# Kernel optimization log

Measured on AMD Instinct MI355X. Metric: run time of the kernel, lower is better.

## Reference

```python
import jax, jax.numpy as jnp
import numpy as np

M, H, D, P = 256, 32, 128, 4096
N = H * D
L = P + M  # total cache length after concat


def setup_inputs() -> dict:
    key = jax.random.key(0)
    ks = jax.random.split(key, 8)
    X = jax.random.normal(ks[0], (M, N), dtype=jnp.float32)
    # projection weights (nn.Linear stores [out, in]; y = x @ W.T)
    Wq = jax.random.normal(ks[1], (N, N), dtype=jnp.float32) * 0.005
    Wk = jax.random.normal(ks[2], (N, N), dtype=jnp.float32) * 0.005
    Wv = jax.random.normal(ks[3], (N, N), dtype=jnp.float32) * 0.005
    cache_K = jax.random.normal(ks[4], (H, P, D), dtype=jnp.float32) * 0.3
    cache_V = jax.random.normal(ks[5], (H, P, D), dtype=jnp.float32) * 0.3
    noise = jax.random.normal(ks[6], (H, M, L), dtype=jnp.float32) * 0.5
    tau = jnp.asarray(2.0, dtype=jnp.float32)
    return {"X": X, "Wq": Wq, "Wk": Wk, "Wv": Wv,
            "cache_K": cache_K, "cache_V": cache_V, "tau": tau, "noise": noise}


def reference(X, Wq, Wk, Wv, cache_K, cache_V, tau, noise):
    # project and split heads: [M, N] -> [H, M, D]
    q = (X @ Wq.T).reshape(M, H, D).transpose(1, 0, 2)
    k = (X @ Wk.T).reshape(M, H, D).transpose(1, 0, 2)
    v = (X @ Wv.T).reshape(M, H, D).transpose(1, 0, 2)
    k_cache = jnp.concatenate([cache_K, k], axis=1)  # [H, L, D]
    v_cache = jnp.concatenate([cache_V, v], axis=1)  # [H, L, D]
    c = jnp.einsum('hmd,hld->hml', q, k_cache)       # [H, M, L]
    # faithful to source: plain exp normalization (no max-subtract), twice
    c_exp = jnp.exp(c)
    c_exp_perturb = jnp.exp((c + noise) / tau)
    c_div = c_exp / jnp.sum(c_exp, axis=2, keepdims=True)
    c_div_perturb = c_exp_perturb / jnp.sum(c_exp_perturb, axis=2, keepdims=True)
    c_out = jnp.sum(c_div_perturb, axis=1)           # [H, L] token scores
    o = jnp.einsum('hml,hld->hmd', c_div, v_cache)   # [H, M, D]
    o2 = o.transpose(1, 0, 2).reshape(M, N)
    return o2, c_out
```

## Files before the change

### kernel.cpp

```cpp
#include <hip/hip_runtime.h>
#include <hip/hip_bf16.h>

#define MM 256
#define HH 32
#define DD 128
#define PP 4096
#define NN 4096
#define LL 4352
#define NSTR 8
#define SPL 4

typedef __attribute__((ext_vector_type(8))) short short8;
typedef __attribute__((ext_vector_type(4))) float f32x4;

__device__ __forceinline__ unsigned short f2bf(float f) {
    union { float f; unsigned u; } x; x.f = f;
    unsigned u = x.u;
    return (unsigned short)((u + 0x7fffu + ((u >> 16) & 1u)) >> 16);
}

__device__ __forceinline__ float bf2f(unsigned short u) {
    union { unsigned u; float f; } x; x.u = ((unsigned)u) << 16;
    return x.f;
}

__device__ __forceinline__ unsigned pkbf(float lo, float hi) {
    unsigned r;
    asm("v_cvt_pk_bf16_f32 %0, %1, %2" : "=v"(r) : "v"(lo), "v"(hi));
    return r;
}

__device__ __forceinline__ short8 pk8(float4 a, float4 b) {
    union { short8 s; unsigned u[4]; } o;
    o.u[0] = pkbf(a.x, a.y); o.u[1] = pkbf(a.z, a.w);
    o.u[2] = pkbf(b.x, b.y); o.u[3] = pkbf(b.z, b.w);
    return o.s;
}

__device__ __forceinline__ f32x4 mfma16(short8 a, short8 b, f32x4 c) {
    return __builtin_amdgcn_mfma_f32_16x16x32_bf16(a, b, c, 0, 0, 0);
}

__global__ __launch_bounds__(256) void conv_x_kernel(const float* __restrict__ src,
                                                     unsigned short* __restrict__ dst) {
    int i = blockIdx.x * 256 + threadIdx.x;
    long in0 = (long)i * 8;
    float4 f0 = *(const float4*)(src + in0);
    float4 f1 = *(const float4*)(src + in0 + 4);
    *(short8*)(dst + in0) = pk8(f0, f1);
}

__global__ __launch_bounds__(256) void conv_k_kernel(const float* __restrict__ src,
                                                     unsigned short* __restrict__ dst) {
    int i = blockIdx.x * 256 + threadIdx.x;
    int h = i >> 16;
    long in0 = (long)i * 8;
    float4 f0 = *(const float4*)(src + in0);
    float4 f1 = *(const float4*)(src + in0 + 4);
    *(short8*)(dst + in0 + (long)h * (LL - PP) * DD) = pk8(f0, f1);
}

__global__ __launch_bounds__(256) void conv_vt_kernel(const float* __restrict__ src,
                                                      unsigned short* __restrict__ dst) {
    __shared__ unsigned short tile[64][65];
    int h = blockIdx.z, l0 = blockIdx.x * 64, d0 = blockIdx.y * 64;
    int t = threadIdx.x;
    int r = t >> 2, c0 = (t & 3) * 16;
    const float* sp = src + ((long)h * PP + l0 + r) * DD + d0 + c0;
#pragma unroll
    for (int j = 0; j < 16; j += 4) {
        float4 f = *(const float4*)(sp + j);
        tile[r][c0 + j + 0] = f2bf(f.x); tile[r][c0 + j + 1] = f2bf(f.y);
        tile[r][c0 + j + 2] = f2bf(f.z); tile[r][c0 + j + 3] = f2bf(f.w);
    }
    __syncthreads();
    unsigned short* dp = dst + ((long)h * DD + d0 + r) * LL + l0 + c0;
    short8 o0, o1;
#pragma unroll
    for (int j = 0; j < 8; ++j) o0[j] = (short)tile[c0 + j][r];
#pragma unroll
    for (int j = 0; j < 8; ++j) o1[j] = (short)tile[c0 + 8 + j][r];
    *(short8*)(dp) = o0;
    *(short8*)(dp + 8) = o1;
}

__device__ __forceinline__ void proj_body(unsigned short* As, unsigned short* Bs,
    const unsigned short* __restrict__ xp, const float* __restrict__ wp,
    int& k0, bool guard, short8 (&ar)[4], float4& b0, float4& b1,
    int arow, int ak0, int brow, int bk0, int mo, int no, int lg, int li,
    f32x4 (&acc)[4][2]) {
#pragma unroll
    for (int c = 0; c < 4; ++c) {
        int kb = (ak0 + c * 8) * 2;
        *(short8*)((char*)As + arow * 128 + (kb ^ ((arow & 7) << 4))) = ar[c];
    }
    {
        short8 v = pk8(b0, b1);
        int kb = bk0 * 2;
        *(short8*)((char*)Bs + brow * 128 + (kb ^ ((brow & 7) << 4))) = v;
    }
    __syncthreads();
    if (guard) {
#pragma unroll
        for (int c = 0; c < 4; ++c) ar[c] = *(const short8*)(xp + k0 + 128 + c * 8);
        b0 = *(const float4*)(wp + k0 + 128);
        b1 = *(const float4*)(wp + k0 + 132);
    }
#pragma unroll
    for (int kk = 0; kk < 2; ++kk) {
        short8 a[4], b[2];
        int kb = kk * 64 + lg * 16;
#pragma unroll
        for (int i = 0; i < 4; ++i) {
            int row = mo + i * 16 + li;
            a[i] = *(const short8*)((char*)As + row * 128 + (kb ^ ((row & 7) << 4)));
        }
#pragma unroll
        for (int j = 0; j < 2; ++j) {
            int row = no + j * 16 + li;
            b[j] = *(const short8*)((char*)Bs + row * 128 + (kb ^ ((row & 7) << 4)));
        }
#pragma unroll
        for (int i = 0; i < 4; ++i)
#pragma unroll
            for (int j = 0; j < 2; ++j)
                acc[i][j] = mfma16(a[i], b[j], acc[i][j]);
    }
    __syncthreads();
    k0 += 64;
}

__global__ __launch_bounds__(512) void proj_gemm_kernel(const unsigned short* __restrict__ xb,
    const float* __restrict__ Wq, const float* __restrict__ Wk, const float* __restrict__ Wv,
    float* __restrict__ qkvfP) {
    const int widx = blockIdx.z;
    const float* __restrict__ W = (widx == 0) ? Wq : (widx == 1 ? Wk : Wv);
    const int n0 = blockIdx.x * 64;
    const int ks = blockIdx.y;
    __shared__ unsigned short As[256 * 64];
    __shared__ unsigned short Bs[64 * 64];
    const int t = threadIdx.x;
    const int wv = t >> 6, lane = t & 63;
    const int lg = lane >> 4, li = lane & 15;
    const int mo = (wv >> 1) * 64, no = (wv & 1) * 32;
    f32x4 acc[4][2];
#pragma unroll
    for (int i = 0; i < 4; ++i)
#pragma unroll
        for (int j = 0; j < 2; ++j) acc[i][j] = (f32x4){0.f, 0.f, 0.f, 0.f};

    const int arow = t >> 1, ak0 = (t & 1) * 32;
    const int brow = t >> 3, bk0 = (t & 7) * 8;
    const unsigned short* xp = xb + (long)arow * NN + ak0;
    const float* wp = W + (long)(n0 + brow) * NN + bk0;

    int k0 = ks * 1024;
    short8 aA[4], aB[4];
    float4 bA0, bA1, bB0, bB1;
#pragma unroll
    for (int c = 0; c < 4; ++c) aA[c] = *(const short8*)(xp + k0 + c * 8);
    bA0 = *(const float4*)(wp + k0);
    bA1 = *(const float4*)(wp + k0 + 4);
#pragma unroll
    for (int c = 0; c < 4; ++c) aB[c] = *(const short8*)(xp + k0 + 64 + c * 8);
    bB0 = *(const float4*)(wp + k0 + 64);
    bB1 = *(const float4*)(wp + k0 + 68);

    for (int it2 = 0; it2 < 8; ++it2) {
        const bool guard = (it2 < 7);
        proj_body(As, Bs, xp, wp, k0, guard, aA, bA0, bA1,
                  arow, ak0, brow, bk0, mo, no, lg, li, acc);
        proj_body(As, Bs, xp, wp, k0, guard, aB, bB0, bB1,
                  arow, ak0, brow, bk0, mo, no, lg, li, acc);
    }

    float* dst = qkvfP + ((long)ks * 3 + widx) * MM * NN;
#pragma unroll
    for (int i = 0; i < 4; ++i)
#pragma unroll
        for (int j = 0; j < 2; ++j)
#pragma unroll
            for (int r = 0; r < 4; ++r) {
                int m = mo + i * 16 + lg * 4 + r;
                int n = n0 + no + j * 16 + li;
                dst[(long)m * NN + n] = acc[i][j][r];
            }
}

__global__ __launch_bounds__(256) void epi_qk_kernel(const float* __restrict__ qkvfP,
    unsigned short* __restrict__ qb, unsigned short* __restrict__ kcat) {
    int i = blockIdx.x * 256 + threadIdx.x;
    int w = i >> 17;
    int r = i & 131071;
    int m = r >> 9;
    int n = (r & 511) * 8;
    float4 f0 = {0,0,0,0}, f1 = {0,0,0,0};
#pragma unroll
    for (int s = 0; s < SPL; ++s) {
        const float* sp = qkvfP + ((long)s * 3 + w) * MM * NN + (long)m * NN + n;
        float4 a0 = *(const float4*)(sp);
        float4 a1 = *(const float4*)(sp + 4);
        f0.x += a0.x; f0.y += a0.y; f0.z += a0.z; f0.w += a0.w;
        f1.x += a1.x; f1.y += a1.y; f1.z += a1.z; f1.w += a1.w;
    }
    short8 v = pk8(f0, f1);
    int h = n >> 7, d = n & 127;
    if (w == 0) *(short8*)(qb + ((long)h * MM + m) * DD + d) = v;
    else        *(short8*)(kcat + ((long)h * LL + PP + m) * DD + d) = v;
}

__global__ __launch_bounds__(256) void epi_v_kernel(const float* __restrict__ qkvfP,
    unsigned short* __restrict__ vT) {
    __shared__ unsigned short tile[64][65];
    int m0 = blockIdx.x * 64, n0 = blockIdx.y * 64;
    int t = threadIdx.x;
    int r = t >> 2, c0 = (t & 3) * 16;
#pragma unroll
    for (int j = 0; j < 16; j += 4) {
        float4 f = {0,0,0,0};
#pragma unroll
        for (int s = 0; s < SPL; ++s) {
            const float* sp = qkvfP + ((long)s * 3 + 2) * MM * NN + (long)(m0 + r) * NN + n0 + c0 + j;
            float4 a = *(const float4*)(sp);
            f.x += a.x; f.y += a.y; f.z += a.z; f.w += a.w;
        }
        tile[r][c0 + j + 0] = f2bf(f.x); tile[r][c0 + j + 1] = f2bf(f.y);
        tile[r][c0 + j + 2] = f2bf(f.z); tile[r][c0 + j + 3] = f2bf(f.w);
    }
    __syncthreads();
    int h = n0 >> 7, d0 = n0 & 127;
    unsigned short* dp = vT + ((long)h * DD + d0 + r) * LL + PP + m0 + c0;
    short8 o0, o1;
#pragma unroll
    for (int j = 0; j < 8; ++j) o0[j] = (short)tile[c0 + j][r];
#pragma unroll
    for (int j = 0; j < 8; ++j) o1[j] = (short)tile[c0 + 8 + j][r];
    *(short8*)(dp) = o0;
    *(short8*)(dp + 8) = o1;
}

__global__ __launch_bounds__(256) void attn_fused_kernel(const unsigned short* __restrict__ qb,
    const unsigned short* __restrict__ kcat, const unsigned short* __restrict__ vT,
    const float* __restrict__ noise, const float* __restrict__ tau,
    float* __restrict__ S1, float* __restrict__ S2,
    unsigned short* __restrict__ e2b, float* __restrict__ owsP) {
    const int bid = blockIdx.x;
    const int swz = (bid & 7) * 128 + (bid >> 3);
    const int mb = swz & 3;
    const int ls = (swz >> 2) & 7;
    const int h  = swz >> 5;
    const int t = threadIdx.x, wv = t >> 6, lane = t & 63;
    const int lg = lane >> 4, li = lane & 15;
    __shared__ unsigned short kbuf[2][32][128];
    __shared__ unsigned short vbuf[2][128][32];
    __shared__ float csbuf[64][32];
    const float inv_tau = 1.0f / tau[0];

    const int mA = mb * 64 + wv * 16 + li;
    const unsigned short* qp = qb + ((long)h * MM + mA) * DD + lg * 8;
    short8 aq[4];
#pragma unroll
    for (int dc = 0; dc < 4; ++dc) aq[dc] = *(const short8*)(qp + dc * 32);

    const int row_l = t >> 2;
    const int col0 = (t & 3) * 8;
    const int mrow_g = mb * 64 + row_l;
    const float* np = noise + ((long)h * MM + mrow_g) * LL + ls * 544 + col0;
    unsigned short* e2p = e2b + ((long)h * MM + mrow_g) * LL + ls * 544 + col0;
    const int csr0 = col0 ^ ((row_l & 7) << 2);
    const int csr1 = (col0 + 4) ^ ((row_l & 7) << 2);
    const int pwB = ((t & 3) ^ (row_l & 3)) * 16;

    const int srow = t >> 3;
    const int kc0 = (t & 7) * 2, kc1 = kc0 + 1;
    const int kwo0 = (kc0 ^ (srow & 7)) * 8, kwo1 = (kc1 ^ (srow & 7)) * 8;
    const unsigned short* ksrc = kcat + ((long)h * LL + ls * 544 + srow) * DD + (t & 7) * 16;
    const int vrow = t >> 1;
    const int vc0 = (t & 1) * 2, vc1 = vc0 + 1;
    const int vwo0 = (vc0 ^ (vrow & 3)) * 8, vwo1 = (vc1 ^ (vrow & 3)) * 8;
    const unsigned short* vsrc = vT + ((long)h * DD + vrow) * LL + ls * 544 + (t & 1) * 16;
    const int vro = (lg ^ (li & 3)) * 8;
    const int prB = (lg ^ (li & 3)) * 16;

    {
        short8 k0 = *(const short8*)(ksrc);
        short8 k1 = *(const short8*)(ksrc + 8);
        *(short8*)(&kbuf[0][srow][kwo0]) = k0;
        *(short8*)(&kbuf[0][srow][kwo1]) = k1;
        short8 v0 = *(const short8*)(vsrc);
        short8 v1 = *(const short8*)(vsrc + 8);
        *(short8*)(&vbuf[0][vrow][vwo0]) = v0;
        *(short8*)(&vbuf[0][vrow][vwo1]) = v1;
    }
    float4 nA0 = *(const float4*)(np);
    float4 nA1 = *(const float4*)(np + 4);
    float4 nB0 = *(const float4*)(np + 32);
    float4 nB1 = *(const float4*)(np + 36);

    f32x4 acc[8];
#pragma unroll
    for (int dt = 0; dt < 8; ++dt) acc[dt] = (f32x4){0.f, 0.f, 0.f, 0.f};
    float s1t = 0.f, s2t = 0.f;
    int cur = 0;
    __syncthreads();

    for (int lc = 0; lc < 17; ++lc) {
        short8 kn0, kn1, vn0, vn1;
        if (lc < 16) {
            const unsigned short* pk = ksrc + (long)((lc + 1) * 32) * DD;
            kn0 = *(const short8*)(pk);
            kn1 = *(const short8*)(pk + 8);
            const unsigned short* pv = vsrc + (lc + 1) * 32;
            vn0 = *(const short8*)(pv);
            vn1 = *(const short8*)(pv + 8);
        }
        f32x4 c0 = (f32x4){0.f,0.f,0.f,0.f}, c1 = (f32x4){0.f,0.f,0.f,0.f};
        __builtin_amdgcn_s_setprio(1);
#pragma unroll
        for (int dc = 0; dc < 4; ++dc) {
            const int kro = ((dc * 4 + lg) ^ (li & 7)) * 8;
            short8 k0 = *(const short8*)(&kbuf[cur][li][kro]);
            short8 k1 = *(const short8*)(&kbuf[cur][16 + li][kro]);
            c0 = mfma16(aq[dc], k0, c0);
            c1 = mfma16(aq[dc], k1, c1);
        }
        __builtin_amdgcn_s_setprio(0);
#pragma unroll
        for (int r = 0; r < 4; ++r) {
            const int csr = wv * 16 + lg * 4 + r;
            const int cx = (csr & 7) << 2;
            csbuf[csr][li ^ cx] = c0[r];
            csbuf[csr][(16 + li) ^ cx] = c1[r];
        }
        float4 cva = *(const float4*)(&csbuf[row_l][csr0]);
        float4 cvb = *(const float4*)(&csbuf[row_l][csr1]);
        float cv[8] = {cva.x, cva.y, cva.z, cva.w, cvb.x, cvb.y, cvb.z, cvb.w};
        float nn[8] = {nA0.x, nA0.y, nA0.z, nA0.w, nA1.x, nA1.y, nA1.z, nA1.w};
        float e1[8], e2[8];
#pragma unroll
        for (int j = 0; j < 8; ++j) {
            e1[j] = __expf(cv[j]);
            e2[j] = __expf((cv[j] + nn[j]) * inv_tau);
            s1t += e1[j];
            s2t += e2[j];
        }
        union { short8 s; unsigned u[4]; } w1, w2;
        w1.u[0] = pkbf(e1[0], e1[1]); w1.u[1] = pkbf(e1[2], e1[3]);
        w1.u[2] = pkbf(e1[4], e1[5]); w1.u[3] = pkbf(e1[6], e1[7]);
        w2.u[0] = pkbf(e2[0], e2[1]); w2.u[1] = pkbf(e2[2], e2[3]);
        w2.u[2] = pkbf(e2[4], e2[5]); w2.u[3] = pkbf(e2[6], e2[7]);
        *(short8*)(e2p + lc * 32) = w2.s;
        *(short8*)((char*)&csbuf[row_l][0] + pwB) = w1.s;
        nA0 = nB0; nA1 = nB1;
        int nx = (lc + 2 < 17) ? (lc + 2) : 16;
        nB0 = *(const float4*)(np + nx * 32);
        nB1 = *(const float4*)(np + nx * 32 + 4);
        {
            short8 pa = *(const short8*)((const char*)&csbuf[wv * 16 + li][0] + prB);
            __builtin_amdgcn_s_setprio(1);
#pragma unroll
            for (int dt = 0; dt < 8; ++dt) {
                short8 bv = *(const short8*)(&vbuf[cur][dt * 16 + li][vro]);
                acc[dt] = mfma16(pa, bv, acc[dt]);
            }
            __builtin_amdgcn_s_setprio(0);
        }
        if (lc < 16) {
            *(short8*)(&kbuf[cur ^ 1][srow][kwo0]) = kn0;
            *(short8*)(&kbuf[cur ^ 1][srow][kwo1]) = kn1;
            *(short8*)(&vbuf[cur ^ 1][vrow][vwo0]) = vn0;
            *(short8*)(&vbuf[cur ^ 1][vrow][vwo1]) = vn1;
        }
        __syncthreads();
        cur ^= 1;
    }

    s1t += __shfl_xor(s1t, 1); s1t += __shfl_xor(s1t, 2);
    s2t += __shfl_xor(s2t, 1); s2t += __shfl_xor(s2t, 2);
    if ((t & 3) == 0) {
        atomicAdd(&S1[h * MM + mrow_g], s1t);
        atomicAdd(&S2[h * MM + mrow_g], s2t);
    }

    const int mD = mb * 64 + wv * 16 + lg * 4;
    float* op = owsP + ((long)ls * HH + h) * MM * DD;
#pragma unroll
    for (int dt = 0; dt < 8; ++dt)
#pragma unroll
        for (int r = 0; r < 4; ++r)
            op[(long)(mD + r) * DD + dt * 16 + li] = acc[dt][r];
}

__global__ __launch_bounds__(256) void finalize_o_kernel(const float* __restrict__ owsP,
    const float* __restrict__ S1, const float* __restrict__ S2,
    float* __restrict__ out, float* __restrict__ invS2) {
    int i = blockIdx.x * 256 + threadIdx.x;
    int hm = i >> 5;
    int d4 = (i & 31) * 4;
    int h = hm >> 8, m = hm & 255;
    float4 s = {0,0,0,0};
#pragma unroll
    for (int st = 0; st < NSTR; ++st) {
        const float4 v = *(const float4*)(owsP + ((long)st * HH * MM + hm) * DD + d4);
        s.x += v.x; s.y += v.y; s.z += v.z; s.w += v.w;
    }
    float inv = 1.0f / S1[hm];
    float4 o;
    o.x = s.x * inv; o.y = s.y * inv; o.z = s.z * inv; o.w = s.w * inv;
    *(float4*)(out + (long)m * NN + h * DD + d4) = o;
    if ((i & 31) == 0) invS2[hm] = 1.0f / S2[hm];
}

__global__ __launch_bounds__(256) void attn_p2_kernel(const unsigned short* __restrict__ e2b,
    const float* __restrict__ invS2, float* __restrict__ cout) {
    const int h = blockIdx.y;
    const int l = blockIdx.x * 256 + threadIdx.x;
    const unsigned short* ep = e2b + (long)h * MM * LL + l;
    const float* is2 = invS2 + h * MM;
    float acc0 = 0.f, acc1 = 0.f, acc2 = 0.f, acc3 = 0.f;
    for (int m = 0; m < MM; m += 4) {
        acc0 += bf2f(__builtin_nontemporal_load(ep + (long)(m + 0) * LL)) * is2[m + 0];
        acc1 += bf2f(__builtin_nontemporal_load(ep + (long)(m + 1) * LL)) * is2[m + 1];
        acc2 += bf2f(__builtin_nontemporal_load(ep + (long)(m + 2) * LL)) * is2[m + 2];
        acc3 += bf2f(__builtin_nontemporal_load(ep + (long)(m + 3) * LL)) * is2[m + 3];
    }
    cout[(long)h * LL + l] = (acc0 + acc1) + (acc2 + acc3);
}

extern "C" void kernel_launch(void* const* d_in, const int* in_sizes, int n_in,
                              void* d_out, int out_size, void* d_ws, size_t ws_size,
                              hipStream_t stream) {
    const float* X     = (const float*)d_in[0];
    const float* Wq    = (const float*)d_in[1];
    const float* Wk    = (const float*)d_in[2];
    const float* Wv    = (const float*)d_in[3];
    const float* cK    = (const float*)d_in[4];
    const float* cV    = (const float*)d_in[5];
    const float* tau   = (const float*)d_in[6];
    const float* noise = (const float*)d_in[7];
    float* out = (float*)d_out;

    char* ws = (char*)d_ws;
    size_t off = 0;
    unsigned short* qb   = (unsigned short*)(ws + off); off += (size_t)HH * MM * DD * 2;
    unsigned short* kcat = (unsigned short*)(ws + off); off += (size_t)HH * LL * DD * 2;
    unsigned short* vT   = (unsigned short*)(ws + off); off += (size_t)HH * LL * DD * 2;
    float* S1    = (float*)(ws + off); off += (size_t)HH * MM * 4;
    float* S2    = (float*)(ws + off); off += (size_t)HH * MM * 4;
    float* invS2 = (float*)(ws + off); off += (size_t)HH * MM * 4;
    float* owsP  = (float*)(ws + off); off += (size_t)NSTR * HH * MM * DD * 4;
    unsigned short* xb = (unsigned short*)(ws + off); off += (size_t)MM * NN * 2;
    float* qkvfP = (float*)(ws + off); off += (size_t)SPL * 3 * MM * NN * 4;
    unsigned short* e2b = (unsigned short*)(ws + off); off += (size_t)HH * MM * LL * 2;

    hipMemsetAsync(S1, 0, 2 * (size_t)HH * MM * 4, stream);

    conv_x_kernel<<<512, 256, 0, stream>>>(X, xb);
    conv_k_kernel<<<8192, 256, 0, stream>>>(cK, kcat);
    conv_vt_kernel<<<dim3(64, 2, 32), 256, 0, stream>>>(cV, vT);
    proj_gemm_kernel<<<dim3(64, SPL, 3), 512, 0, stream>>>(xb, Wq, Wk, Wv, qkvfP);
    epi_qk_kernel<<<1024, 256, 0, stream>>>(qkvfP, qb, kcat);
    epi_v_kernel<<<dim3(4, 64), 256, 0, stream>>>(qkvfP, vT);
    attn_fused_kernel<<<1024, 256, 0, stream>>>(qb, kcat, vT, noise, tau, S1, S2, e2b, owsP);
    finalize_o_kernel<<<1024, 256, 0, stream>>>(owsP, S1, S2, out, invS2);
    attn_p2_kernel<<<dim3(17, 32), 256, 0, stream>>>(e2b, invS2, out + (size_t)MM * NN);
}
```

Before: 245.4 us.

## Double-buffer LDS in projection GEMM with 128-row M tiles and block swizzle

```diff
diff --git a/kernel.cpp b/kernel.cpp
--- a/kernel.cpp
+++ b/kernel.cpp
@@ -84,28 +84,8 @@
     *(short8*)(dp + 8) = o1;
 }
 
-__device__ __forceinline__ void proj_body(unsigned short* As, unsigned short* Bs,
-    const unsigned short* __restrict__ xp, const float* __restrict__ wp,
-    int& k0, bool guard, short8 (&ar)[4], float4& b0, float4& b1,
-    int arow, int ak0, int brow, int bk0, int mo, int no, int lg, int li,
-    f32x4 (&acc)[4][2]) {
-#pragma unroll
-    for (int c = 0; c < 4; ++c) {
-        int kb = (ak0 + c * 8) * 2;
-        *(short8*)((char*)As + arow * 128 + (kb ^ ((arow & 7) << 4))) = ar[c];
-    }
-    {
-        short8 v = pk8(b0, b1);
-        int kb = bk0 * 2;
-        *(short8*)((char*)Bs + brow * 128 + (kb ^ ((brow & 7) << 4))) = v;
-    }
-    __syncthreads();
-    if (guard) {
-#pragma unroll
-        for (int c = 0; c < 4; ++c) ar[c] = *(const short8*)(xp + k0 + 128 + c * 8);
-        b0 = *(const float4*)(wp + k0 + 128);
-        b1 = *(const float4*)(wp + k0 + 132);
-    }
+__device__ __forceinline__ void mfma_phase(const unsigned short* As, const unsigned short* Bs,
+    int mo, int no, int lg, int li, f32x4 (&acc)[4][2]) {
 #pragma unroll
     for (int kk = 0; kk < 2; ++kk) {
         short8 a[4], b[2];
@@ -113,12 +93,12 @@
 #pragma unroll
         for (int i = 0; i < 4; ++i) {
             int row = mo + i * 16 + li;
-            a[i] = *(const short8*)((char*)As + row * 128 + (kb ^ ((row & 7) << 4)));
+            a[i] = *(const short8*)((const char*)As + row * 128 + (kb ^ ((row & 7) << 4)));
         }
 #pragma unroll
         for (int j = 0; j < 2; ++j) {
             int row = no + j * 16 + li;
-            b[j] = *(const short8*)((char*)Bs + row * 128 + (kb ^ ((row & 7) << 4)));
+            b[j] = *(const short8*)((const char*)Bs + row * 128 + (kb ^ ((row & 7) << 4)));
         }
 #pragma unroll
         for (int i = 0; i < 4; ++i)
@@ -126,19 +106,20 @@
             for (int j = 0; j < 2; ++j)
                 acc[i][j] = mfma16(a[i], b[j], acc[i][j]);
     }
-    __syncthreads();
-    k0 += 64;
-}
-
-__global__ __launch_bounds__(512) void proj_gemm_kernel(const unsigned short* __restrict__ xb,
+}
+
+__global__ __launch_bounds__(256) void proj_gemm_kernel(const unsigned short* __restrict__ xb,
     const float* __restrict__ Wq, const float* __restrict__ Wk, const float* __restrict__ Wv,
     float* __restrict__ qkvfP) {
     const int widx = blockIdx.z;
     const float* __restrict__ W = (widx == 0) ? Wq : (widx == 1 ? Wk : Wv);
-    const int n0 = blockIdx.x * 64;
+    const int x = blockIdx.x;
+    const int sx = (x & 7) * 16 + (x >> 3);
+    const int mt = sx & 1;
+    const int n0 = (sx >> 1) * 64;
     const int ks = blockIdx.y;
-    __shared__ unsigned short As[256 * 64];
-    __shared__ unsigned short Bs[64 * 64];
+    __shared__ unsigned short As[2][128 * 64];
+    __shared__ unsigned short Bs[2][64 * 64];
     const int t = threadIdx.x;
     const int wv = t >> 6, lane = t & 63;
     const int lg = lane >> 4, li = lane & 15;
@@ -150,29 +131,54 @@
         for (int j = 0; j < 2; ++j) acc[i][j] = (f32x4){0.f, 0.f, 0.f, 0.f};
 
     const int arow = t >> 1, ak0 = (t & 1) * 32;
-    const int brow = t >> 3, bk0 = (t & 7) * 8;
-    const unsigned short* xp = xb + (long)arow * NN + ak0;
+    const int brow = t >> 2, bk0 = (t & 3) * 16;
+    const unsigned short* xp = xb + (long)(mt * 128 + arow) * NN + ak0;
     const float* wp = W + (long)(n0 + brow) * NN + bk0;
-
-    int k0 = ks * 1024;
-    short8 aA[4], aB[4];
-    float4 bA0, bA1, bB0, bB1;
-#pragma unroll
-    for (int c = 0; c < 4; ++c) aA[c] = *(const short8*)(xp + k0 + c * 8);
-    bA0 = *(const float4*)(wp + k0);
-    bA1 = *(const float4*)(wp + k0 + 4);
-#pragma unroll
-    for (int c = 0; c < 4; ++c) aB[c] = *(const short8*)(xp + k0 + 64 + c * 8);
-    bB0 = *(const float4*)(wp + k0 + 64);
-    bB1 = *(const float4*)(wp + k0 + 68);
+    const int kbase = ks * 1024;
+
+    short8 ar[4];
+    float4 b0, b1, b2, b3;
+
+#define PLOAD(k) do { \
+    _Pragma("unroll") \
+    for (int c_ = 0; c_ < 4; ++c_) ar[c_] = *(const short8*)(xp + (k) + c_ * 8); \
+    b0 = *(const float4*)(wp + (k));      b1 = *(const float4*)(wp + (k) + 4); \
+    b2 = *(const float4*)(wp + (k) + 8);  b3 = *(const float4*)(wp + (k) + 12); \
+} while (0)
+
+#define PSTORE(buf) do { \
+    unsigned short* As_ = As[buf]; unsigned short* Bs_ = Bs[buf]; \
+    _Pragma("unroll") \
+    for (int c_ = 0; c_ < 4; ++c_) { \
+        int kb_ = (ak0 + c_ * 8) * 2; \
+        *(short8*)((char*)As_ + arow * 128 + (kb_ ^ ((arow & 7) << 4))) = ar[c_]; \
+    } \
+    { \
+        short8 v0_ = pk8(b0, b1), v1_ = pk8(b2, b3); \
+        int kb0_ = bk0 * 2, kb1_ = (bk0 + 8) * 2; \
+        *(short8*)((char*)Bs_ + brow * 128 + (kb0_ ^ ((brow & 7) << 4))) = v0_; \
+        *(short8*)((char*)Bs_ + brow * 128 + (kb1_ ^ ((brow & 7) << 4))) = v1_; \
+    } \
+} while (0)
+
+    PLOAD(kbase);
+    PSTORE(0);
+    PLOAD(kbase + 64);
+    __syncthreads();
 
     for (int it2 = 0; it2 < 8; ++it2) {
-        const bool guard = (it2 < 7);
-        proj_body(As, Bs, xp, wp, k0, guard, aA, bA0, bA1,
-                  arow, ak0, brow, bk0, mo, no, lg, li, acc);
-        proj_body(As, Bs, xp, wp, k0, guard, aB, bB0, bB1,
-                  arow, ak0, brow, bk0, mo, no, lg, li, acc);
-    }
+        const int e = it2 * 2;
+        PSTORE(1);
+        if (e < 14) PLOAD(kbase + (e + 2) * 64);
+        mfma_phase(As[0], Bs[0], mo, no, lg, li, acc);
+        __syncthreads();
+        if (e + 2 < 16) PSTORE(0);
+        if (e + 3 < 16) PLOAD(kbase + (e + 3) * 64);
+        mfma_phase(As[1], Bs[1], mo, no, lg, li, acc);
+        __syncthreads();
+    }
+#undef PLOAD
+#undef PSTORE
 
     float* dst = qkvfP + ((long)ks * 3 + widx) * MM * NN;
 #pragma unroll
@@ -181,7 +187,7 @@
         for (int j = 0; j < 2; ++j)
 #pragma unroll
             for (int r = 0; r < 4; ++r) {
-                int m = mo + i * 16 + lg * 4 + r;
+                int m = mt * 128 + mo + i * 16 + lg * 4 + r;
                 int n = n0 + no + j * 16 + li;
                 dst[(long)m * NN + n] = acc[i][j][r];
             }
@@ -458,7 +464,7 @@
     conv_x_kernel<<<512, 256, 0, stream>>>(X, xb);
     conv_k_kernel<<<8192, 256, 0, stream>>>(cK, kcat);
     conv_vt_kernel<<<dim3(64, 2, 32), 256, 0, stream>>>(cV, vT);
-    proj_gemm_kernel<<<dim3(64, SPL, 3), 512, 0, stream>>>(xb, Wq, Wk, Wv, qkvfP);
+    proj_gemm_kernel<<<dim3(128, SPL, 3), 256, 0, stream>>>(xb, Wq, Wk, Wv, qkvfP);
     epi_qk_kernel<<<1024, 256, 0, stream>>>(qkvfP, qb, kcat);
     epi_v_kernel<<<dim3(4, 64), 256, 0, stream>>>(qkvfP, vT);
     attn_fused_kernel<<<1024, 256, 0, stream>>>(qb, kcat, vT, noise, tau, S1, S2, e2b, owsP);
```

Result: slower. 255.5 us (+4.1%).
